# Kernel optimization log

Measured on AMD Instinct MI355X. Metric: run time of the kernel, lower is better.

## Reference

```python
import jax, jax.numpy as jnp
import numpy as np

H = 512          # hidden_dim
T = 80           # future_length
M = 6            # num_modes
OD = 2           # output_dim
B = 2048         # batch
TEMP = 1.2


def _lin_params(key, out_dim, in_dim, scale=0.02):
    kw, kb = jax.random.split(key)
    W = jax.random.normal(kw, (out_dim, in_dim), jnp.float32) * scale
    b = jax.random.normal(kb, (out_dim,), jnp.float32) * scale
    return W, b


def _per_mode(key, out_dim, in_dim, scale=0.02):
    ks = jax.random.split(key, M)
    Ws, bs = [], []
    for k in ks:
        W, b = _lin_params(k, out_dim, in_dim, scale)
        Ws.append(W); bs.append(b)
    return jnp.stack(Ws), jnp.stack(bs)


def setup_inputs() -> dict:
    key = jax.random.key(0)
    ks = jax.random.split(key, 20)
    inp = {}
    inp['composed_features'] = jax.random.normal(ks[0], (B, H), jnp.float32)
    # mode_decoders: Linear(H,2H) ReLU [Dropout] Linear(2H,H) ReLU [Dropout] Linear(H,H)
    inp['md_W1'], inp['md_b1'] = _per_mode(ks[1], 2 * H, H)
    inp['md_W2'], inp['md_b2'] = _per_mode(ks[2], H, 2 * H)
    inp['md_W3'], inp['md_b3'] = _per_mode(ks[3], H, H)
    # initial_hidden_projections: Linear(H, 2H)
    inp['ih_W'], inp['ih_b'] = _per_mode(ks[4], 2 * H, H)
    # time_projection (shared): Linear(1, H//2) ReLU Linear(H//2, H)
    inp['tp_W1'], inp['tp_b1'] = _lin_params(ks[5], H // 2, 1)
    inp['tp_W2'], inp['tp_b2'] = _lin_params(ks[6], H, H // 2)
    # feedback_projections: Linear(OD, H//2)
    inp['fb_W'], inp['fb_b'] = _per_mode(ks[7], H // 2, OD)
    # LSTM (2 layers, torch gate order i,f,g,o), per mode
    inp['l0_Wih'], inp['l0_bih'] = _per_mode(ks[8], 4 * H, H)
    inp['l0_Whh'], inp['l0_bhh'] = _per_mode(ks[9], 4 * H, H)
    inp['l1_Wih'], inp['l1_bih'] = _per_mode(ks[10], 4 * H, H)
    inp['l1_Whh'], inp['l1_bhh'] = _per_mode(ks[11], 4 * H, H)
    # output_projections: Linear(H,H) ReLU [Dropout] Linear(H,OD)
    inp['op_W1'], inp['op_b1'] = _per_mode(ks[12], H, H)
    inp['op_W2'], inp['op_b2'] = _per_mode(ks[13], OD, H)
    # confidence_head (shared): Linear(H, H//2) ReLU [Dropout] Linear(H//2, M)
    inp['cf_W1'], inp['cf_b1'] = _lin_params(ks[14], H // 2, H)
    inp['cf_W2'], inp['cf_b2'] = _lin_params(ks[15], M, H // 2)
    return inp


def _lstm_cell(x, h, c, Wih, Whh, bih, bhh):
    g = x @ Wih.T + h @ Whh.T + (bih + bhh)
    i, f, gg, o = jnp.split(g, 4, axis=-1)
    c_new = jax.nn.sigmoid(f) * c + jax.nn.sigmoid(i) * jnp.tanh(gg)
    h_new = jax.nn.sigmoid(o) * jnp.tanh(c_new)
    return h_new, c_new


def _forward(composed_features,
             md_W1, md_b1, md_W2, md_b2, md_W3, md_b3,
             ih_W, ih_b, tp_W1, tp_b1, tp_W2, tp_b2,
             fb_W, fb_b,
             l0_Wih, l0_bih, l0_Whh, l0_bhh,
             l1_Wih, l1_bih, l1_Whh, l1_bhh,
             op_W1, op_b1, op_W2, op_b2,
             cf_W1, cf_b1, cf_W2, cf_b2):
    x = composed_features
    bsz = x.shape[0]
    # shared time embeddings for all steps: [T, H]
    t_norm = (jnp.arange(T, dtype=jnp.float32) / (T - 1))[:, None]
    time_embs = jax.nn.relu(t_norm @ tp_W1.T + tp_b1) @ tp_W2.T + tp_b2

    def run_mode(mW1, mb1, mW2, mb2, mW3, mb3, iW, ib, fW, fb,
                 W0i, b0i, W0h, b0h, W1i, b1i, W1h, b1h,
                 oW1, ob1, oW2, ob2):
        # mode decoder (dropout = identity in eval)
        mf = jax.nn.relu(x @ mW1.T + mb1)
        mf = jax.nn.relu(mf @ mW2.T + mb2)
        mf = mf @ mW3.T + mb3                      # [B, H]
        init = x @ iW.T + ib                       # [B, 2H]
        h0 = init[:, :H]; c0 = init[:, H:]
        carry = (h0, c0, h0, c0, jnp.zeros((bsz, OD), x.dtype))
        pad = H - H // 2

        def step(carry, te_t):
            h0, c0, h1, c1, prev = carry
            fb_half = prev @ fW.T + fb             # [B, H//2]
            fb_full = jnp.pad(fb_half, ((0, 0), (0, pad)))
            xin = mf + 0.5 * te_t[None, :] + 0.3 * fb_full
            h0, c0 = _lstm_cell(xin, h0, c0, W0i, W0h, b0i, b0h)
            h1, c1 = _lstm_cell(h0, h1, c1, W1i, W1h, b1i, b1h)
            out = jax.nn.relu(h1 @ oW1.T + ob1) @ oW2.T + ob2  # [B, OD]
            return (h0, c0, h1, c1, out), out

        _, outs = jax.lax.scan(step, carry, time_embs)   # [T, B, OD]
        traj = jnp.transpose(outs, (1, 0, 2))            # [B, T, OD]
        return traj.at[:, 0, :].set(0.0)

    trajs = jax.vmap(run_mode)(md_W1, md_b1, md_W2, md_b2, md_W3, md_b3,
                               ih_W, ih_b, fb_W, fb_b,
                               l0_Wih, l0_bih, l0_Whh, l0_bhh,
                               l1_Wih, l1_bih, l1_Whh, l1_bhh,
                               op_W1, op_b1, op_W2, op_b2)  # [M, B, T, OD]
    trajectories = jnp.transpose(trajs, (1, 0, 2, 3))       # [B, M, T, OD]
    logits = jax.nn.relu(x @ cf_W1.T + cf_b1) @ cf_W2.T + cf_b2  # [B, M]
    confidences = jax.nn.softmax(logits / TEMP, axis=-1)
    return trajectories, confidences, logits


def reference(composed_features,
              md_W1, md_b1, md_W2, md_b2, md_W3, md_b3,
              ih_W, ih_b, tp_W1, tp_b1, tp_W2, tp_b2,
              fb_W, fb_b,
              l0_Wih, l0_bih, l0_Whh, l0_bhh,
              l1_Wih, l1_bih, l1_Whh, l1_bhh,
              op_W1, op_b1, op_W2, op_b2,
              cf_W1, cf_b1, cf_W2, cf_b2):
    return _forward(composed_features,
                    md_W1, md_b1, md_W2, md_b2, md_W3, md_b3,
                    ih_W, ih_b, tp_W1, tp_b1, tp_W2, tp_b2,
                    fb_W, fb_b,
                    l0_Wih, l0_bih, l0_Whh, l0_bhh,
                    l1_Wih, l1_bih, l1_Whh, l1_bhh,
                    op_W1, op_b1, op_W2, op_b2,
                    cf_W1, cf_b1, cf_W2, cf_b2)
```

## Files before the change

### kernel.cpp

```cpp
#include <hip/hip_runtime.h>
#include <cstdint>

typedef __bf16 bf16;
typedef __bf16 bf16x8 __attribute__((ext_vector_type(8)));
typedef float f32x4 __attribute__((ext_vector_type(4)));

#define DI __device__ __forceinline__

#define BATCH 2048
#define HD 512
#define NM 6

DI float rcp_(float x){ return __builtin_amdgcn_rcpf(x); }
DI float sigmoidf_(float x){ return rcp_(1.0f + __expf(-x)); }
DI float tanhf_(float x){
  float a = __expf(-2.0f * fabsf(x));
  float t = (1.0f - a) * rcp_(1.0f + a);
  return __builtin_copysignf(t, x);
}

DI void gload16(const bf16* g, char* l){
  __builtin_amdgcn_global_load_lds(
    (const __attribute__((address_space(1))) void*)g,
    (__attribute__((address_space(3))) void*)l, 16, 0, 0);
}

__global__ void k_diag(float* out, float wsmb){
  if (threadIdx.x == 0 && blockIdx.x == 0) out[0] = wsmb * 1.0e6f;
}

template<bool GATES, bool DUAL>
__global__ void k_pack(bf16* __restrict__ dst, const float* __restrict__ s1,
                       const float* __restrict__ s2, int K, int NROW, int ksplit)
{
  long idx = (long)blockIdx.x * 256 + threadIdx.x;
  int kper = K >> 3;
  int k0 = (int)(idx % kper) * 8;
  long rest = idx / kper;
  int p = (int)(rest % NROW);
  int mm = (int)(rest / NROW);
  int r;
  if (GATES){
    int nb2 = p >> 7, hi = (p >> 6) & 1, g = (p >> 4) & 3, jl = p & 15;
    r = g * 512 + nb2 * 32 + hi * 16 + jl;
  } else r = p;
  const float* src;
  if (DUAL){
    if (k0 >= ksplit) src = s2 + ((long)mm * NROW + r) * ksplit + (k0 - ksplit);
    else              src = s1 + ((long)mm * NROW + r) * ksplit + k0;
  } else {
    src = s1 + ((long)mm * NROW + r) * K + k0;
  }
  f32x4 v0 = *(const f32x4*)(src);
  f32x4 v1 = *(const f32x4*)(src + 4);
  bf16x8 o;
  #pragma unroll
  for (int k = 0; k < 4; ++k){ o[k] = (bf16)v0[k]; o[4+k] = (bf16)v1[k]; }
  *(bf16x8*)(dst + ((long)mm * NROW + p) * K + k0) = o;
}

__global__ void k_temb(bf16* tembb, const float* tpW1, const float* tpb1,
                       const float* tpW2, const float* tpb2)
{
  int t = blockIdx.x; int tid = threadIdx.x;
  __shared__ float rq[256];
  float tn = (t < 80) ? (float)t / 79.0f : 0.0f;
  rq[tid] = fmaxf(tn * tpW1[tid] + tpb1[tid], 0.0f);
  __syncthreads();
  for (int d = tid; d < 512; d += 256){
    float s = tpb2[d];
    const float* w = tpW2 + d * 256;
    for (int q = 0; q < 256; ++q) s += rq[q] * w[q];
    tembb[t * 512 + d] = (bf16)((t < 80) ? 0.5f * s : 0.0f);
  }
}

__global__ void k_biases(float* bias0p, float* bias1p,
                         const float* l0bih, const float* l0bhh,
                         const float* l1bih, const float* l1bhh,
                         const float* l0Wih, const float* fbb)
{
  int idx = blockIdx.x * 256 + threadIdx.x;
  int m = idx >> 11, p = idx & 2047;
  int nb2 = p >> 7, hi = (p >> 6) & 1, g = (p >> 4) & 3, jl = p & 15;
  int r = g * 512 + nb2 * 32 + hi * 16 + jl;
  bias1p[idx] = l1bih[m * 2048 + r] + l1bhh[m * 2048 + r];
  const float* wrow = l0Wih + ((long)m * 2048 + r) * 512;
  const float* fb = fbb + m * 256;
  float acc = 0.0f;
  for (int q = 0; q < 256; ++q) acc += fb[q] * wrow[q];
  bias0p[idx] = l0bih[m * 2048 + r] + l0bhh[m * 2048 + r] + 0.3f * acc;
}

__global__ void k_feffp(float* feffp, const float* fbW, const float* l0Wih)
{
  int idx = blockIdx.x * 256 + threadIdx.x;
  int p = idx & 2047, o = (idx >> 11) & 1, m = idx >> 12;
  int nb2 = p >> 7, hi = (p >> 6) & 1, g = (p >> 4) & 3, jl = p & 15;
  int r = g * 512 + nb2 * 32 + hi * 16 + jl;
  const float* wrow = l0Wih + ((long)m * 2048 + r) * 512;
  float acc = 0.0f;
  for (int q = 0; q < 256; ++q) acc += fbW[((long)m * 256 + q) * 2 + o] * wrow[q];
  feffp[((long)m * 2 + o) * 2048 + p] = 0.3f * acc;
}

__global__ void k_zero(float* part, float* traj)
{
  int i = blockIdx.x * 256 + threadIdx.x;
  part[i] = 0.0f;
  if (i < 24576){
    int od = i & 1, mm = (i >> 1) % 6, b = i / 12;
    traj[b * 960 + mm * 160 + od] = 0.0f;
  }
}

__global__ void k_logits(const bf16* lt1, const float* cfW2, const float* cfb2,
                         float* conf, float* logitsOut)
{
  int b = blockIdx.x * 256 + threadIdx.x;
  float acc[6];
  #pragma unroll
  for (int mm = 0; mm < 6; ++mm) acc[mm] = cfb2[mm];
  for (int q = 0; q < 256; ++q){
    float xv = (float)lt1[b * 256 + q];
    #pragma unroll
    for (int mm = 0; mm < 6; ++mm) acc[mm] += xv * cfW2[mm * 256 + q];
  }
  float mx = acc[0];
  #pragma unroll
  for (int mm = 1; mm < 6; ++mm) mx = fmaxf(mx, acc[mm]);
  float e[6], s = 0.0f;
  #pragma unroll
  for (int mm = 0; mm < 6; ++mm){ e[mm] = __expf((acc[mm] - mx) * (1.0f / 1.2f)); s += e[mm]; }
  float inv = 1.0f / s;
  #pragma unroll
  for (int mm = 0; mm < 6; ++mm){
    logitsOut[b * 6 + mm] = acc[mm];
    conf[b * 6 + mm] = e[mm] * inv;
  }
}

__global__ void k_red(const float* part, const float* opb2, float* traj)
{
  int i = blockIdx.x * 256 + threadIdx.x;
  int m = i >> 11, b = i & 2047;
  const float* pp = part + (long)i * 8;
  float o0 = pp[0] + pp[2] + pp[4] + pp[6] + opb2[m * 2];
  float o1 = pp[1] + pp[3] + pp[5] + pp[7] + opb2[m * 2 + 1];
  traj[(long)b * 960 + m * 160 + 158] = o0;
  traj[(long)b * 960 + m * 160 + 159] = o1;
}

struct GArgs {
  const bf16* A1; const bf16* A2; const bf16* Bw;
  long a1_ms, a2_ms, b_ms;
  int a_ld, K, ksplit, NBt, MBt, tprev;
  const float* biasf; long bias_ms;
  bf16* out_bf; long out_ms; int out_ld;
  float* out_f; long outf_ms;
  const bf16* baseb; long baseb_ms;
  const float* temb; long temb_ms;
  const float* feff; long feff_ms;
  const float* prevp;
  const float* ob2;
  const float* w2;
  float* part;
  float* cbuf; long c_ms;
  bf16* hout; long h_ms;
  bf16* hout2; float* cbuf2;
};

enum { EP_RELU = 0, EP_BF16 = 1, EP_F32 = 2, EP_INIT = 3, EP_LSTM = 4, EP_OUT = 5 };

template<int EP, bool SPLIT, bool FB>
__global__ __launch_bounds__(256, 2)
void gemm_k(GArgs a)
{
  __shared__ __attribute__((aligned(16))) char smem[33792];
  char* As = smem;
  char* Bs = smem + 16384;
  float* Gf = (float*)smem;

  const int id  = blockIdx.x;
  const int id2 = (id & 7) * ((int)gridDim.x >> 3) + (id >> 3);
  const int per = a.MBt * a.NBt;
  const int m   = id2 / per;
  const int rem = id2 - m * per;
  const int mb  = rem / a.NBt;
  const int nb  = rem - mb * a.NBt;

  const int tid = threadIdx.x;
  const int lane = tid & 63;
  const int wid  = tid >> 6;
  const int wr = wid >> 1, wc = wid & 1;

  const bf16* A1m = a.A1 + (long)m * a.a1_ms;
  const bf16* A2m = SPLIT ? (a.A2 + (long)m * a.a2_ms) : nullptr;
  const bf16* Bm  = a.Bw + (long)m * a.b_ms + (long)nb * 128 * a.K;

  f32x4 acc[4][4];
  if constexpr (EP == EP_LSTM && FB){
    const int jl_ = lane & 15;
    const int qr_ = lane >> 4;
    const bf16* bb0 = a.baseb + (long)m * a.baseb_ms
                      + (long)nb * 128 + wc * 64 + jl_;
    #pragma unroll
    for (int i = 0; i < 4; ++i)
      #pragma unroll
      for (int q = 0; q < 4; ++q){
        long b = mb * 128 + wr * 64 + i * 16 + qr_ * 4 + q;
        #pragma unroll
        for (int g = 0; g < 4; ++g)
          acc[i][g][q] = (float)bb0[b * 2048 + g * 16];
      }
  } else {
    #pragma unroll
    for (int i = 0; i < 4; ++i)
      #pragma unroll
      for (int j = 0; j < 4; ++j) acc[i][j] = f32x4{0.f, 0.f, 0.f, 0.f};
  }

  const int rl = lane >> 3;
  const int sg = (lane & 7) ^ rl;
  const bf16* a1B[4]; const bf16* a2B[4]; const bf16* bB[4];
  char* ldA[4]; char* ldB[4];
  #pragma unroll
  for (int c = 0; c < 4; ++c){
    int rt = (wid * 4 + c) * 8 + rl;
    a1B[c] = A1m + (long)(mb * 128 + rt) * a.a_ld + sg * 8;
    if (SPLIT) a2B[c] = A2m + (long)(mb * 128 + rt) * a.a_ld + sg * 8;
    bB[c]  = Bm + (long)rt * a.K + sg * 8;
    ldA[c] = As + (wid * 4 + c) * 1024;
    ldB[c] = Bs + (wid * 4 + c) * 1024;
  }
  auto STAGE = [&](int kb){
    int kcol = kb << 6;
    if (SPLIT && kcol >= a.ksplit){
      int kl = kcol - a.ksplit;
      #pragma unroll
      for (int c = 0; c < 4; ++c){ gload16(a2B[c] + kl, ldA[c]); gload16(bB[c] + kcol, ldB[c]); }
    } else {
      #pragma unroll
      for (int c = 0; c < 4; ++c){ gload16(a1B[c] + kcol, ldA[c]); gload16(bB[c] + kcol, ldB[c]); }
    }
  };

  const int nk = a.K >> 6;
  STAGE(0);
  for (int kb = 0; kb < nk; ++kb){
    __syncthreads();
    bf16x8 af[2][4], bg[2][4];
    #pragma unroll
    for (int ks = 0; ks < 2; ++ks){
      #pragma unroll
      for (int f = 0; f < 4; ++f){
        int rr = wr * 64 + f * 16 + (lane & 15);
        int kB = ks * 64 + ((lane >> 4) << 4);
        af[ks][f] = *(const bf16x8*)(As + rr * 128 + (kB ^ ((rr & 7) << 4)));
        int rb = wc * 64 + f * 16 + (lane & 15);
        bg[ks][f] = *(const bf16x8*)(Bs + rb * 128 + (kB ^ ((rb & 7) << 4)));
      }
    }
    __syncthreads();
    if (kb + 1 < nk) STAGE(kb + 1);
    #pragma unroll
    for (int ks = 0; ks < 2; ++ks)
      #pragma unroll
      for (int i = 0; i < 4; ++i)
        #pragma unroll
        for (int j = 0; j < 4; ++j)
          acc[i][j] = __builtin_amdgcn_mfma_f32_16x16x32_bf16(af[ks][i], bg[ks][j], acc[i][j], 0, 0, 0);
  }

  if constexpr (EP == EP_LSTM){
    const int jl = lane & 15;
    const int qr = lane >> 4;
    const int jh = nb * 32 + wc * 16 + jl;
    const long pbase = (long)nb * 128 + wc * 64 + jl;
    float addv[4], f0v[4], f1v[4];
    #pragma unroll
    for (int g = 0; g < 4; ++g){
      long p = pbase + g * 16;
      if constexpr (FB){
        addv[g] = a.temb[(long)m * a.temb_ms + p];
        f0v[g]  = a.feff[(long)m * a.feff_ms + p];
        f1v[g]  = a.feff[(long)m * a.feff_ms + 2048 + p];
      } else {
        addv[g] = a.biasf[(long)m * a.bias_ms + p];
      }
    }
    float* pvs = (float*)smem;
    if constexpr (FB){
      if (tid < 128){
        float pv0 = 0.f, pv1 = 0.f;
        long b = mb * 128 + tid;
        if (a.tprev >= 0){
          const float* pp = a.prevp + ((long)m * 2048 + b) * 8;
          f32x4 pa = *(const f32x4*)(pp);
          f32x4 pb = *(const f32x4*)(pp + 4);
          pv0 = pa[0] + pa[2] + pb[0] + pb[2] + a.ob2[m * 2];
          pv1 = pa[1] + pa[3] + pb[1] + pb[3] + a.ob2[m * 2 + 1];
        }
        pvs[tid * 2]     = pv0;
        pvs[tid * 2 + 1] = pv1;
        if (nb == 0 && a.tprev >= 1){
          a.out_f[b * 960 + m * 160 + a.tprev * 2 + 0] = pv0;
          a.out_f[b * 960 + m * 160 + a.tprev * 2 + 1] = pv1;
        }
      }
      __syncthreads();
    }
    float* cb = a.cbuf + (long)m * a.c_ms + jh;
    bf16*  hb = a.hout + (long)m * a.h_ms + jh;
    #pragma unroll
    for (int i = 0; i < 4; ++i){
      #pragma unroll
      for (int q = 0; q < 4; ++q){
        int r = wr * 64 + i * 16 + qr * 4 + q;
        int b = mb * 128 + r;
        float pv0 = 0.f, pv1 = 0.f;
        if constexpr (FB){ pv0 = pvs[r * 2]; pv1 = pvs[r * 2 + 1]; }
        float g4[4];
        #pragma unroll
        for (int g = 0; g < 4; ++g){
          float v = acc[i][g][q] + addv[g];
          if constexpr (FB) v += pv0 * f0v[g] + pv1 * f1v[g];
          g4[g] = v;
        }
        long ro = (long)b * HD;
        float ci = sigmoidf_(g4[0]), cf = sigmoidf_(g4[1]);
        float cg = tanhf_(g4[2]),    co = sigmoidf_(g4[3]);
        float cn = cf * cb[ro] + ci * cg;
        cb[ro] = cn;
        hb[ro] = (bf16)(co * tanhf_(cn));
      }
    }
    return;
  }

  if constexpr (EP == EP_OUT){
    __syncthreads();
    float* ps = (float*)smem;
    int colbase = wc * 64 + (lane & 15);
    float bv[4], w0v[4], w1v[4];
    #pragma unroll
    for (int j = 0; j < 4; ++j){
      int p = nb * 128 + colbase + j * 16;
      bv[j]  = a.biasf[(long)m * a.bias_ms + p];
      w0v[j] = a.w2[(long)m * 1024 + p];
      w1v[j] = a.w2[(long)m * 1024 + 512 + p];
    }
    #pragma unroll
    for (int i = 0; i < 4; ++i)
      #pragma unroll
      for (int q = 0; q < 4; ++q){
        float s0 = 0.f, s1 = 0.f;
        #pragma unroll
        for (int j = 0; j < 4; ++j){
          float v = fmaxf(acc[i][j][q] + bv[j], 0.0f);
          s0 += v * w0v[j]; s1 += v * w1v[j];
        }
        #pragma unroll
        for (int o2 = 1; o2 < 16; o2 <<= 1){ s0 += __shfl_xor(s0, o2); s1 += __shfl_xor(s1, o2); }
        if ((lane & 15) == 0){
          int row = wr * 64 + i * 16 + ((lane >> 4) << 2) + q;
          ps[row * 4 + wc * 2 + 0] = s0;
          ps[row * 4 + wc * 2 + 1] = s1;
        }
      }
    __syncthreads();
    if (tid < 128){
      int b = mb * 128 + tid;
      float o0 = ps[tid * 4 + 0] + ps[tid * 4 + 2];
      float o1 = ps[tid * 4 + 1] + ps[tid * 4 + 3];
      a.part[((long)m * 2048 + b) * 8 + nb * 2 + 0] = o0;
      a.part[((long)m * 2048 + b) * 8 + nb * 2 + 1] = o1;
    }
    return;
  }

  #pragma unroll 1
  for (int ph = 0; ph < 2; ++ph){
    __syncthreads();
    if (wc == ph){
      #pragma unroll
      for (int i = 0; i < 4; ++i)
        #pragma unroll
        for (int j = 0; j < 4; ++j)
          #pragma unroll
          for (int q = 0; q < 4; ++q){
            int rr = wr * 64 + i * 16 + ((lane >> 4) << 2) + q;
            int cc = j * 16 + (lane & 15);
            Gf[rr * 66 + cc] = acc[i][j][q];
          }
    }
    __syncthreads();

    #pragma unroll 1
    for (int it = 0; it < 4; ++it){
      int u = it * 256 + tid;
      int r = u >> 3, cg = u & 7;
      int b = mb * 128 + r;
      int p0 = nb * 128 + ph * 64 + cg * 8;
      float v[8];
      #pragma unroll
      for (int k2 = 0; k2 < 8; ++k2){
        v[k2] = Gf[r * 66 + cg * 8 + k2];
        if (a.biasf) v[k2] += a.biasf[(long)m * a.bias_ms + p0 + k2];
        if constexpr (EP == EP_RELU) v[k2] = fmaxf(v[k2], 0.0f);
      }
      if constexpr (EP == EP_F32){
        float* dst = a.out_f + (long)m * a.outf_ms + (long)b * a.out_ld + p0;
        #pragma unroll
        for (int k2 = 0; k2 < 8; ++k2) dst[k2] = v[k2];
      } else if constexpr (EP == EP_INIT){
        if (p0 < HD){
          bf16x8 ov;
          #pragma unroll
          for (int k2 = 0; k2 < 8; ++k2) ov[k2] = (bf16)v[k2];
          *(bf16x8*)(a.hout  + (long)m * a.h_ms + (long)b * HD + p0) = ov;
          *(bf16x8*)(a.hout2 + (long)m * a.h_ms + (long)b * HD + p0) = ov;
        } else {
          int p1 = p0 - HD;
          float* d1 = a.cbuf  + (long)m * a.c_ms + (long)b * HD + p1;
          float* d2 = a.cbuf2 + (long)m * a.c_ms + (long)b * HD + p1;
          #pragma unroll
          for (int k2 = 0; k2 < 8; ++k2){ d1[k2] = v[k2]; d2[k2] = v[k2]; }
        }
      } else {
        bf16x8 ov;
        #pragma unroll
        for (int k2 = 0; k2 < 8; ++k2) ov[k2] = (bf16)v[k2];
        *(bf16x8*)(a.out_bf + (long)m * a.out_ms + (long)b * a.out_ld + p0) = ov;
      }
    }
  }
}

extern "C" void kernel_launch(void* const* d_in, const int* in_sizes, int n_in,
                              void* d_out, int out_size, void* d_ws, size_t ws_size,
                              hipStream_t stream)
{
  (void)in_sizes; (void)n_in; (void)out_size;
  const float* X     = (const float*)d_in[0];
  const float* mdW1  = (const float*)d_in[1];
  const float* mdb1  = (const float*)d_in[2];
  const float* mdW2  = (const float*)d_in[3];
  const float* mdb2  = (const float*)d_in[4];
  const float* mdW3  = (const float*)d_in[5];
  const float* mdb3  = (const float*)d_in[6];
  const float* ihW   = (const float*)d_in[7];
  const float* ihb   = (const float*)d_in[8];
  const float* tpW1  = (const float*)d_in[9];
  const float* tpb1  = (const float*)d_in[10];
  const float* tpW2  = (const float*)d_in[11];
  const float* tpb2  = (const float*)d_in[12];
  const float* fbW   = (const float*)d_in[13];
  const float* fbb   = (const float*)d_in[14];
  const float* l0Wih = (const float*)d_in[15];
  const float* l0bih = (const float*)d_in[16];
  const float* l0Whh = (const float*)d_in[17];
  const float* l0bhh = (const float*)d_in[18];
  const float* l1Wih = (const float*)d_in[19];
  const float* l1bih = (const float*)d_in[20];
  const float* l1Whh = (const float*)d_in[21];
  const float* l1bhh = (const float*)d_in[22];
  const float* opW1  = (const float*)d_in[23];
  const float* opb1  = (const float*)d_in[24];
  const float* opW2  = (const float*)d_in[25];
  const float* opb2  = (const float*)d_in[26];
  const float* cfW1  = (const float*)d_in[27];
  const float* cfb1  = (const float*)d_in[28];
  const float* cfW2  = (const float*)d_in[29];
  const float* cfb2  = (const float*)d_in[30];
  float* out = (float*)d_out;

  const size_t NEED = 211009536;
  if (ws_size < NEED){
    k_diag<<<1, 64, 0, stream>>>(out, (float)(ws_size >> 20));
    return;
  }
  char* ws = (char*)d_ws;
  const long BH = (long)BATCH * HD;

  bf16*  Wp0     = (bf16*) (ws + 0);
  bf16*  Wp1     = (bf16*) (ws + 12582912);
  bf16*  WpO     = (bf16*) (ws + 37748736);
  bf16*  base0p  = (bf16*) (ws + 40894464);
  float* tembW0p = (float*)(ws + 91226112);
  float* bias1p  = (float*)(ws + 97517568);
  float* Feffp   = (float*)(ws + 97566720);
  char*  REG     =          ws + 97763328;
  bf16*  h0b     = (bf16*) (REG + 0);
  bf16*  h1b     = (bf16*) (REG + 25165824);
  float* c0      = (float*)(REG + 50331648);
  float* c1      = (float*)(REG + 75497472);
  char*  MREG    =          ws + 198426624;

  bf16*  W0ip    = (bf16*) (REG + 0);
  bf16*  mdW1p   = (bf16*) (REG + 12582912);
  bf16*  mdW2p   = (bf16*) (REG + 18874368);
  bf16*  mdW3p   = (bf16*) (REG + 25165824);
  bf16*  tembb   = (bf16*) (REG + 28311552);
  float* bias0p  = (float*)(REG + 28442624);
  bf16*  lt1     = (bf16*) (REG + 28491776);
  bf16*  t1buf   = (bf16*) (REG + 29540352);
  bf16*  t2buf   = (bf16*) (REG + 54706176);
  bf16*  mfbuf   = (bf16*) (REG + 67289088);
  bf16*  xb      = (bf16*) (MREG + 0);
  bf16*  ihWp    = (bf16*) (MREG + 2097152);
  bf16*  cfW1p   = (bf16*) (MREG + 8388608);
  float* part    = (float*)(MREG + 8650752);

  k_pack<false,false><<<dim3(512),  256, 0, stream>>>(xb,    X,     nullptr, 512,  2048, 512);
  k_pack<true ,false><<<dim3(3072), 256, 0, stream>>>(Wp0,   l0Whh, nullptr, 512,  2048, 512);
  k_pack<true ,false><<<dim3(3072), 256, 0, stream>>>(W0ip,  l0Wih, nullptr, 512,  2048, 512);
  k_pack<true ,true ><<<dim3(6144), 256, 0, stream>>>(Wp1,   l1Wih, l1Whh,   1024, 2048, 512);
  k_pack<false,false><<<dim3(768),  256, 0, stream>>>(WpO,   opW1,  nullptr, 512,  512,  512);
  k_pack<false,false><<<dim3(1536), 256, 0, stream>>>(mdW1p, mdW1,  nullptr, 512,  1024, 512);
  k_pack<false,false><<<dim3(1536), 256, 0, stream>>>(mdW2p, mdW2,  nullptr, 1024, 512,  1024);
  k_pack<false,false><<<dim3(768),  256, 0, stream>>>(mdW3p, mdW3,  nullptr, 512,  512,  512);
  k_pack<false,false><<<dim3(1536), 256, 0, stream>>>(ihWp,  ihW,   nullptr, 512,  1024, 512);
  k_pack<false,false><<<dim3(64),   256, 0, stream>>>(cfW1p, cfW1,  nullptr, 512,  256,  512);

  k_temb  <<<dim3(128), 256, 0, stream>>>(tembb, tpW1, tpb1, tpW2, tpb2);
  k_biases<<<dim3(48),  256, 0, stream>>>(bias0p, bias1p, l0bih, l0bhh, l1bih, l1bhh, l0Wih, fbb);
  k_feffp <<<dim3(96),  256, 0, stream>>>(Feffp, fbW, l0Wih);
  k_zero  <<<dim3(384), 256, 0, stream>>>(part, out);

  { GArgs g{}; g.A1 = xb; g.a1_ms = 0; g.a_ld = 512; g.Bw = mdW1p; g.b_ms = (long)1024*512;
    g.K = 512; g.ksplit = 512; g.NBt = 8; g.MBt = 16; g.biasf = mdb1; g.bias_ms = 1024;
    g.out_bf = t1buf; g.out_ms = (long)2048*1024; g.out_ld = 1024;
    gemm_k<EP_RELU,false,false><<<dim3(16*8*6), 256, 0, stream>>>(g); }
  { GArgs g{}; g.A1 = t1buf; g.a1_ms = (long)2048*1024; g.a_ld = 1024; g.Bw = mdW2p; g.b_ms = (long)512*1024;
    g.K = 1024; g.ksplit = 1024; g.NBt = 4; g.MBt = 16; g.biasf = mdb2; g.bias_ms = 512;
    g.out_bf = t2buf; g.out_ms = BH; g.out_ld = 512;
    gemm_k<EP_RELU,false,false><<<dim3(16*4*6), 256, 0, stream>>>(g); }
  { GArgs g{}; g.A1 = t2buf; g.a1_ms = BH; g.a_ld = 512; g.Bw = mdW3p; g.b_ms = (long)512*512;
    g.K = 512; g.ksplit = 512; g.NBt = 4; g.MBt = 16; g.biasf = mdb3; g.bias_ms = 512;
    g.out_bf = mfbuf; g.out_ms = BH; g.out_ld = 512;
    gemm_k<EP_BF16,false,false><<<dim3(16*4*6), 256, 0, stream>>>(g); }
  { GArgs g{}; g.A1 = tembb; g.a1_ms = 0; g.a_ld = 512; g.Bw = W0ip; g.b_ms = (long)2048*512;
    g.K = 512; g.ksplit = 512; g.NBt = 16; g.MBt = 1; g.biasf = nullptr;
    g.out_f = tembW0p; g.outf_ms = (long)128*2048; g.out_ld = 2048;
    gemm_k<EP_F32,false,false><<<dim3(1*16*6), 256, 0, stream>>>(g); }
  { GArgs g{}; g.A1 = mfbuf; g.a1_ms = BH; g.a_ld = 512; g.Bw = W0ip; g.b_ms = (long)2048*512;
    g.K = 512; g.ksplit = 512; g.NBt = 16; g.MBt = 16; g.biasf = bias0p; g.bias_ms = 2048;
    g.out_bf = base0p; g.out_ms = (long)2048*2048; g.out_ld = 2048;
    gemm_k<EP_BF16,false,false><<<dim3(16*16*6), 256, 0, stream>>>(g); }
  { GArgs g{}; g.A1 = xb; g.a1_ms = 0; g.a_ld = 512; g.Bw = cfW1p; g.b_ms = 0;
    g.K = 512; g.ksplit = 512; g.NBt = 2; g.MBt = 16; g.biasf = cfb1; g.bias_ms = 0;
    g.out_bf = lt1; g.out_ms = 0; g.out_ld = 256;
    gemm_k<EP_RELU,false,false><<<dim3(16*2*1), 256, 0, stream>>>(g); }
  k_logits<<<dim3(8), 256, 0, stream>>>(lt1, cfW2, cfb2, out + 1966080, out + 1966080 + 12288);
  { GArgs g{}; g.A1 = xb; g.a1_ms = 0; g.a_ld = 512; g.Bw = ihWp; g.b_ms = (long)1024*512;
    g.K = 512; g.ksplit = 512; g.NBt = 8; g.MBt = 16; g.biasf = ihb; g.bias_ms = 1024;
    g.hout = h0b; g.h_ms = BH; g.hout2 = h1b; g.cbuf = c0; g.c_ms = BH; g.cbuf2 = c1;
    gemm_k<EP_INIT,false,false><<<dim3(16*8*6), 256, 0, stream>>>(g); }

  for (int t = 0; t < 80; ++t){
    int cur = t & 1, nxt = cur ^ 1;
    { GArgs g{}; g.A1 = h0b + (size_t)cur * 6 * BH; g.a1_ms = BH; g.a_ld = 512;
      g.Bw = Wp0; g.b_ms = (long)2048*512; g.K = 512; g.ksplit = 512; g.NBt = 16; g.MBt = 16;
      g.tprev = t - 1;
      g.baseb = base0p; g.baseb_ms = (long)2048*2048;
      g.temb = tembW0p + (long)t * 2048; g.temb_ms = (long)128*2048;
      g.feff = Feffp; g.feff_ms = 4096;
      g.prevp = part; g.ob2 = opb2; g.out_f = out;
      g.cbuf = c0; g.c_ms = BH;
      g.hout = h0b + (size_t)nxt * 6 * BH; g.h_ms = BH;
      gemm_k<EP_LSTM,false,true><<<dim3(16*16*6), 256, 0, stream>>>(g); }
    { GArgs g{}; g.A1 = h0b + (size_t)nxt * 6 * BH; g.A2 = h1b + (size_t)cur * 6 * BH;
      g.a1_ms = BH; g.a2_ms = BH; g.a_ld = 512;
      g.Bw = Wp1; g.b_ms = (long)2048*1024; g.K = 1024; g.ksplit = 512; g.NBt = 16; g.MBt = 16;
      g.biasf = bias1p; g.bias_ms = 2048;
      g.cbuf = c1; g.c_ms = BH;
      g.hout = h1b + (size_t)nxt * 6 * BH; g.h_ms = BH;
      gemm_k<EP_LSTM,true,false><<<dim3(16*16*6), 256, 0, stream>>>(g); }
    { GArgs g{}; g.A1 = h1b + (size_t)nxt * 6 * BH; g.a1_ms = BH; g.a_ld = 512;
      g.Bw = WpO; g.b_ms = (long)512*512; g.K = 512; g.ksplit = 512; g.NBt = 4; g.MBt = 16;
      g.biasf = opb1; g.bias_ms = 512;
      g.w2 = opW2; g.part = part;
      gemm_k<EP_OUT,false,false><<<dim3(16*4*6), 256, 0, stream>>>(g); }
  }
  k_red<<<dim3(48), 256, 0, stream>>>(part, opb2, out);
}
```

Baseline: 9.380 ms.

## Halve GEMM K-tile to 32 and raise occupancy to three blocks per CU

Cuts the per-iteration K slice from 64 to 32 columns, which halves the fragment registers held per k-step and shrinks the staged A/B tiles to 8 KB each. It reworks the LDS swizzle for 64-byte rows and raises the launch bound from 2 to 3 blocks per CU, aiming for more occupancy to hide latency in the serial LSTM GEMMs. The price is twice as many K iterations, each with two barriers and less MFMA work between them. The shared array stays 33792 bytes, presumably because the epilogue still uses it, so LDS may be what caps occupancy.

Result: slower. 10.17 ms (+8.5%).

```diff
diff --git a/kernel.cpp b/kernel.cpp
--- a/kernel.cpp
+++ b/kernel.cpp
@@ -173,12 +173,12 @@
 enum { EP_RELU = 0, EP_BF16 = 1, EP_F32 = 2, EP_INIT = 3, EP_LSTM = 4, EP_OUT = 5 };
 
 template<int EP, bool SPLIT, bool FB>
-__global__ __launch_bounds__(256, 2)
+__global__ __launch_bounds__(256, 3)
 void gemm_k(GArgs a)
 {
   __shared__ __attribute__((aligned(16))) char smem[33792];
   char* As = smem;
-  char* Bs = smem + 16384;
+  char* Bs = smem + 8192;
   float* Gf = (float*)smem;
 
   const int id  = blockIdx.x;
@@ -220,56 +220,54 @@
       for (int j = 0; j < 4; ++j) acc[i][j] = f32x4{0.f, 0.f, 0.f, 0.f};
   }
 
-  const int rl = lane >> 3;
-  const int sg = (lane & 7) ^ rl;
-  const bf16* a1B[4]; const bf16* a2B[4]; const bf16* bB[4];
-  char* ldA[4]; char* ldB[4];
+  const int rl = lane >> 2;
+  const int sl = lane & 3;
+  const int sg = sl ^ ((rl ^ (rl >> 2)) & 3);
+  const bf16* a1B[2]; const bf16* a2B[2]; const bf16* bB[2];
+  char* ldA[2]; char* ldB[2];
   #pragma unroll
-  for (int c = 0; c < 4; ++c){
-    int rt = (wid * 4 + c) * 8 + rl;
+  for (int c = 0; c < 2; ++c){
+    int u  = wid * 2 + c;
+    int rt = u * 16 + rl;
     a1B[c] = A1m + (long)(mb * 128 + rt) * a.a_ld + sg * 8;
     if (SPLIT) a2B[c] = A2m + (long)(mb * 128 + rt) * a.a_ld + sg * 8;
     bB[c]  = Bm + (long)rt * a.K + sg * 8;
-    ldA[c] = As + (wid * 4 + c) * 1024;
-    ldB[c] = Bs + (wid * 4 + c) * 1024;
+    ldA[c] = As + u * 1024;
+    ldB[c] = Bs + u * 1024;
   }
   auto STAGE = [&](int kb){
-    int kcol = kb << 6;
+    int kcol = kb << 5;
     if (SPLIT && kcol >= a.ksplit){
       int kl = kcol - a.ksplit;
       #pragma unroll
-      for (int c = 0; c < 4; ++c){ gload16(a2B[c] + kl, ldA[c]); gload16(bB[c] + kcol, ldB[c]); }
+      for (int c = 0; c < 2; ++c){ gload16(a2B[c] + kl, ldA[c]); gload16(bB[c] + kcol, ldB[c]); }
     } else {
       #pragma unroll
-      for (int c = 0; c < 4; ++c){ gload16(a1B[c] + kcol, ldA[c]); gload16(bB[c] + kcol, ldB[c]); }
+      for (int c = 0; c < 2; ++c){ gload16(a1B[c] + kcol, ldA[c]); gload16(bB[c] + kcol, ldB[c]); }
     }
   };
 
-  const int nk = a.K >> 6;
+  const int nk = a.K >> 5;
+  const int jl_r = lane & 15;
+  const int kslot = ((lane >> 4) ^ ((jl_r ^ (jl_r >> 2)) & 3)) << 4;
   STAGE(0);
   for (int kb = 0; kb < nk; ++kb){
     __syncthreads();
-    bf16x8 af[2][4], bg[2][4];
-    #pragma unroll
-    for (int ks = 0; ks < 2; ++ks){
-      #pragma unroll
-      for (int f = 0; f < 4; ++f){
-        int rr = wr * 64 + f * 16 + (lane & 15);
-        int kB = ks * 64 + ((lane >> 4) << 4);
-        af[ks][f] = *(const bf16x8*)(As + rr * 128 + (kB ^ ((rr & 7) << 4)));
-        int rb = wc * 64 + f * 16 + (lane & 15);
-        bg[ks][f] = *(const bf16x8*)(Bs + rb * 128 + (kB ^ ((rb & 7) << 4)));
-      }
+    bf16x8 af[4], bg[4];
+    #pragma unroll
+    for (int f = 0; f < 4; ++f){
+      int rr = wr * 64 + f * 16 + jl_r;
+      af[f] = *(const bf16x8*)(As + rr * 64 + kslot);
+      int rb = wc * 64 + f * 16 + jl_r;
+      bg[f] = *(const bf16x8*)(Bs + rb * 64 + kslot);
     }
     __syncthreads();
     if (kb + 1 < nk) STAGE(kb + 1);
     #pragma unroll
-    for (int ks = 0; ks < 2; ++ks)
-      #pragma unroll
-      for (int i = 0; i < 4; ++i)
-        #pragma unroll
-        for (int j = 0; j < 4; ++j)
-          acc[i][j] = __builtin_amdgcn_mfma_f32_16x16x32_bf16(af[ks][i], bg[ks][j], acc[i][j], 0, 0, 0);
+    for (int i = 0; i < 4; ++i)
+      #pragma unroll
+      for (int j = 0; j < 4; ++j)
+        acc[i][j] = __builtin_amdgcn_mfma_f32_16x16x32_bf16(af[i], bg[j], acc[i][j], 0, 0, 0);
   }
 
   if constexpr (EP == EP_LSTM){
```
